# Performance work log

Measured on AMD Instinct MI355X. Metric: run time of the kernel, lower is better.

Reference implementation:

```python
import jax, jax.numpy as jnp
import numpy as np

BN_EPS = 1e-5


def setup_inputs() -> dict:
    key = jax.random.key(0)
    ks = jax.random.split(key, 20)
    B, C, T, H, W = 32, 1024, 4, 14, 14
    Ci = C // 2  # inter_channels = 512
    s = lambda fan: 1.0 / np.sqrt(fan)
    inp = {
        "x_body": jax.random.normal(ks[0], (B, C, T, H, W), jnp.float32),
        "x_face": jax.random.normal(ks[1], (B, 512), jnp.float32),
        # 1x1x1 conv projections of the non-local block
        "Wg": jax.random.normal(ks[2], (Ci, C), jnp.float32) * s(C),
        "bg": jnp.zeros((Ci,), jnp.float32),
        "Wth": jax.random.normal(ks[3], (Ci, C), jnp.float32) * s(C),
        "bth": jnp.zeros((Ci,), jnp.float32),
        "Wph": jax.random.normal(ks[4], (Ci, C), jnp.float32) * s(C),
        "bph": jnp.zeros((Ci,), jnp.float32),
        # output projection W + BatchNorm (inference stats)
        "Ww": jax.random.normal(ks[5], (C, Ci), jnp.float32) * s(Ci),
        "bw": jnp.zeros((C,), jnp.float32),
        "bn_gamma": jax.random.normal(ks[6], (C,), jnp.float32) * 0.1 + 1.0,
        "bn_beta": jax.random.normal(ks[7], (C,), jnp.float32) * 0.1,
        "bn_mean": jax.random.normal(ks[8], (C,), jnp.float32) * 0.1,
        "bn_var": jax.random.uniform(ks[9], (C,), jnp.float32, 0.5, 1.5),
        # FC head
        "W1": jax.random.normal(ks[10], (512, 1024), jnp.float32) * s(1024),
        "b1": jnp.zeros((512,), jnp.float32),
        "W2": jax.random.normal(ks[11], (2, 1024), jnp.float32) * s(1024),
        "b2": jnp.zeros((2,), jnp.float32),
    }
    return inp


def reference(x_body, x_face, Wg, bg, Wth, bth, Wph, bph, Ww, bw,
              bn_gamma, bn_beta, bn_mean, bn_var, W1, b1, W2, b2):
    B, C, T, H, W = x_body.shape
    N = T * H * W  # 784 spatial-temporal positions
    xf = x_body.reshape(B, C, N)

    # embedded-Gaussian non-local block (1x1x1 convs == channel matmuls)
    g_x = jnp.einsum('ic,bcn->bin', Wg, xf) + bg[:, None]      # [B,Ci,N]
    theta = jnp.einsum('ic,bcn->bni', Wth, xf) + bth[None, None, :]  # [B,N,Ci]
    phi = jnp.einsum('ic,bcn->bin', Wph, xf) + bph[:, None]    # [B,Ci,N]
    f = jnp.einsum('bni,bim->bnm', theta, phi)                 # [B,N,N]
    attn = jax.nn.softmax(f, axis=-1)
    y = jnp.einsum('bnm,bim->bin', attn, g_x)                  # [B,Ci,N]

    # W conv back to C channels + BatchNorm (eval) + residual
    wy = jnp.einsum('ci,bin->bcn', Ww, y) + bw[:, None]        # [B,C,N]
    inv = bn_gamma / jnp.sqrt(bn_var + BN_EPS)
    wy = wy * inv[:, None] + (bn_beta - bn_mean * inv)[:, None]
    z = wy + xf                                                # residual

    # adaptive avg pool to (1,1,1) == mean over N, then FC head
    pooled = jnp.mean(z, axis=-1)                              # [B,C]
    h = pooled @ W1.T + b1                                     # [B,512]
    cat = jnp.concatenate([h, x_face], axis=1)                 # [B,1024]
    out = cat @ W2.T + b2                                      # [B,2]
    return out
```

## Files before the change

### kernel.cpp

```cpp
#include <hip/hip_runtime.h>

typedef unsigned short u16;
typedef float f32x4 __attribute__((ext_vector_type(4)));
typedef short s16x8 __attribute__((ext_vector_type(8)));

#define NB 32
#define NC 1024
#define CI 512
#define NN 784
#define NPAD 896
#define M3 1536

#define OFF_XBT   0ull
#define OFF_WCAT  58720256ull
#define OFF_PROJ  61865984ull
#define OFF_ABAR  138985472ull
#define OFF_XBAR  139085824ull
#define OFF_YBAR  0ull
#define OFF_POOL  65536ull
#define OFF_H     196608ull

__device__ __forceinline__ u16 f2bf(float x) {
    union { float f; unsigned u; } v; v.f = x;
    unsigned r = v.u + 0x7fffu + ((v.u >> 16) & 1u);
    return (u16)(r >> 16);
}
__device__ __forceinline__ float bf2f(u16 h) {
    union { unsigned u; float f; } v; v.u = ((unsigned)h) << 16;
    return v.f;
}
__device__ __forceinline__ void gload16(const u16* g, u16* l) {
    __builtin_amdgcn_global_load_lds(
        (const __attribute__((address_space(1))) unsigned int*)(const void*)g,
        (__attribute__((address_space(3))) unsigned int*)(void*)l,
        16, 0, 0);
}
__device__ __forceinline__ float wred_sum(float s) {
    #pragma unroll
    for (int o = 32; o; o >>= 1) s += __shfl_xor(s, o);
    return s;
}

__global__ void k_cast_w(const float* __restrict__ Wth, const float* __restrict__ Wph,
                         const float* __restrict__ Wg, u16* __restrict__ Wcat) {
    int T = blockIdx.x * 256 + threadIdx.x;
    int e = T * 4;
    int row = e >> 10, col = e & 1023;
    const float* src = (row < 512) ? (Wth + (size_t)row * 1024)
                     : (row < 1024) ? (Wph + (size_t)(row - 512) * 1024)
                                    : (Wg + (size_t)(row - 1024) * 1024);
    float4 v = *(const float4*)(src + col);
    ushort4 o;
    o.x = f2bf(v.x); o.y = f2bf(v.y); o.z = f2bf(v.z); o.w = f2bf(v.w);
    *(ushort4*)(Wcat + e) = o;
}

__global__ void k_tcast(const float* __restrict__ xb, u16* __restrict__ xbT,
                        float* __restrict__ xbar) {
    __shared__ float tile[32][33];
    int b = blockIdx.z, c0 = blockIdx.y * 32, n0 = blockIdx.x * 32;
    int t = threadIdx.x, j = t & 31, r0 = t >> 5;
    const float* xp = xb + ((size_t)b * NC + c0) * NN;
    #pragma unroll
    for (int rr = r0; rr < 32; rr += 8) {
        int n = n0 + j;
        tile[rr][j] = (n < NN) ? xp[(size_t)rr * NN + n] : 0.f;
    }
    __syncthreads();
    if (t < 32) {
        float s = 0.f;
        #pragma unroll
        for (int q = 0; q < 32; ++q) s += tile[t][q];
        atomicAdd(&xbar[b * NC + c0 + t], s);
    }
    #pragma unroll
    for (int rr = r0; rr < 32; rr += 8) {
        int n = n0 + rr;
        if (n < NN) xbT[((size_t)b * NPAD + n)* NC + c0 + j] = f2bf(tile[j][rr]);
    }
}

__global__ __launch_bounds__(256) void k_gemm(
        const u16* __restrict__ xbT, const u16* __restrict__ Wcat,
        const float* __restrict__ bth, const float* __restrict__ bph,
        const float* __restrict__ bg, u16* __restrict__ proj) {
    __shared__ u16 At[128 * 32];
    __shared__ u16 Bt[128 * 32];
    int b = blockIdx.z, nt = blockIdx.x, mt = blockIdx.y;
    int t = threadIdx.x, w = t >> 6, l = t & 63;
    int wn = w & 1, wm = w >> 1;
    const u16* Ag = xbT + (size_t)b * NPAD * NC + (size_t)nt * 128 * NC;
    const u16* Bg = Wcat + (size_t)mt * 128 * NC;
    int lrow = l >> 2;
    int cg = ((l & 3) ^ ((l >> 3) & 3)) * 8;
    int lc = l & 15, lr = l >> 4;
    int sA = (lr ^ ((lc >> 1) & 3)) * 8;
    f32x4 acc[4][4] = {};
    for (int kt = 0; kt < 32; ++kt) {
        int k0 = kt * 32;
        int s0 = w * 2, s1 = w * 2 + 1;
        gload16(Ag + (size_t)(s0 * 16 + lrow) * NC + k0 + cg, At + s0 * 512);
        gload16(Ag + (size_t)(s1 * 16 + lrow) * NC + k0 + cg, At + s1 * 512);
        gload16(Bg + (size_t)(s0 * 16 + lrow) * NC + k0 + cg, Bt + s0 * 512);
        gload16(Bg + (size_t)(s1 * 16 + lrow) * NC + k0 + cg, Bt + s1 * 512);
        __syncthreads();
        s16x8 af[4], bf_[4];
        #pragma unroll
        for (int i = 0; i < 4; ++i)
            af[i] = *(const s16x8*)&At[(wn * 64 + i * 16 + lc) * 32 + sA];
        #pragma unroll
        for (int jj = 0; jj < 4; ++jj)
            bf_[jj] = *(const s16x8*)&Bt[(wm * 64 + jj * 16 + lc) * 32 + sA];
        #pragma unroll
        for (int i = 0; i < 4; ++i)
            #pragma unroll
            for (int jj = 0; jj < 4; ++jj)
                acc[i][jj] = __builtin_amdgcn_mfma_f32_16x16x32_bf16(af[i], bf_[jj], acc[i][jj], 0, 0, 0);
        __syncthreads();
    }
    size_t ob = (size_t)b * NN * M3;
    #pragma unroll
    for (int jj = 0; jj < 4; ++jj) {
        int m = mt * 128 + wm * 64 + jj * 16 + lc;
        float bv = (m < 512) ? bth[m] : (m < 1024) ? bph[m - 512] : bg[m - 1024];
        #pragma unroll
        for (int i = 0; i < 4; ++i) {
            int nbase = nt * 128 + wn * 64 + i * 16 + lr * 4;
            #pragma unroll
            for (int r = 0; r < 4; ++r) {
                int n = nbase + r;
                if (n < NN) proj[ob + (size_t)n * M3 + m] = f2bf(acc[i][jj][r] + bv);
            }
        }
    }
}

__global__ __launch_bounds__(256) void k_attn(const u16* __restrict__ proj,
                                              float* __restrict__ abar) {
    extern __shared__ char smem[];
    u16* th   = (u16*)smem;
    float* S  = (float*)(smem + 33280);
    float* rmax = (float*)(smem + 134144);
    float* rinv = rmax + 32;
    int nb = blockIdx.x, b = blockIdx.y;
    int n0 = nb * 32;
    int t = threadIdx.x, w = t >> 6, l = t & 63;
    const u16* pb = proj + (size_t)b * NN * M3;
    {
        int row = t >> 3, kb = (t & 7) * 64;
        const u16* src = pb + (size_t)(n0 + row) * M3 + kb;
        u16* dst = th + row * 520 + kb;
        #pragma unroll
        for (int q = 0; q < 8; ++q) *(s16x8*)(dst + q * 8) = *(const s16x8*)(src + q * 8);
    }
    __syncthreads();
    int lc = l & 15, lr = l >> 4, ko = lr * 8;
    for (int mtile = w; mtile < 49; mtile += 4) {
        f32x4 a0 = {0.f, 0.f, 0.f, 0.f}, a1 = {0.f, 0.f, 0.f, 0.f};
        const u16* ph = pb + 512 + (size_t)(mtile * 16 + lc) * M3;
        #pragma unroll
        for (int ks = 0; ks < 16; ++ks) {
            s16x8 bfrag = *(const s16x8*)(ph + ks * 32 + ko);
            s16x8 t0 = *(const s16x8*)(th + lc * 520 + ks * 32 + ko);
            s16x8 t1 = *(const s16x8*)(th + (16 + lc) * 520 + ks * 32 + ko);
            a0 = __builtin_amdgcn_mfma_f32_16x16x32_bf16(t0, bfrag, a0, 0, 0, 0);
            a1 = __builtin_amdgcn_mfma_f32_16x16x32_bf16(t1, bfrag, a1, 0, 0, 0);
        }
        int m = mtile * 16 + lc;
        #pragma unroll
        for (int r = 0; r < 4; ++r) {
            S[(lr * 4 + r) * 788 + m]        = a0[r];
            S[(16 + lr * 4 + r) * 788 + m]   = a1[r];
        }
    }
    __syncthreads();
    for (int r = w; r < 32; r += 4) {
        const float* Sr = S + r * 788;
        float mx = -1e30f;
        for (int m = l; m < NN; m += 64) mx = fmaxf(mx, Sr[m]);
        #pragma unroll
        for (int o = 32; o; o >>= 1) mx = fmaxf(mx, __shfl_xor(mx, o));
        float sm = 0.f;
        for (int m = l; m < NN; m += 64) sm += __expf(Sr[m] - mx);
        sm = wred_sum(sm);
        if (l == 0) { rmax[r] = mx; rinv[r] = 1.f / sm; }
    }
    __syncthreads();
    int nvalid = NN - n0; if (nvalid > 32) nvalid = 32;
    for (int m = t; m < NN; m += 256) {
        float cs = 0.f;
        for (int r = 0; r < nvalid; ++r) cs += __expf(S[r * 788 + m] - rmax[r]) * rinv[r];
        atomicAdd(&abar[b * NN + m], cs);
    }
}

__global__ __launch_bounds__(256) void k_ybar(const u16* __restrict__ proj,
                                              const float* __restrict__ abar,
                                              float* __restrict__ ybar) {
    __shared__ float part[4][CI];
    __shared__ float ab[49];
    int b = blockIdx.y, m0 = blockIdx.x * 49;
    int t = threadIdx.x, r = t >> 6, l = t & 63;
    if (t < 49) ab[t] = abar[b * NN + m0 + t];
    __syncthreads();
    const u16* g = proj + (size_t)b * NN * M3 + 1024;
    float acc[8] = {};
    for (int m = m0 + r; m < m0 + 49; m += 4) {
        float a = ab[m - m0];
        s16x8 v = *(const s16x8*)(g + (size_t)m * M3 + l * 8);
        #pragma unroll
        for (int j = 0; j < 8; ++j) acc[j] += a * bf2f((u16)v[j]);
    }
    #pragma unroll
    for (int j = 0; j < 8; ++j) part[r][l * 8 + j] = acc[j];
    __syncthreads();
    if (r == 0) {
        #pragma unroll
        for (int j = 0; j < 8; ++j) {
            int i = l * 8 + j;
            atomicAdd(&ybar[b * CI + i],
                      part[0][i] + part[1][i] + part[2][i] + part[3][i]);
        }
    }
}

__global__ __launch_bounds__(256) void k_pooled(const float* __restrict__ ybar,
        const float* __restrict__ xbar,
        const float* __restrict__ Ww, const float* __restrict__ bw,
        const float* __restrict__ gamma, const float* __restrict__ beta,
        const float* __restrict__ mean, const float* __restrict__ var,
        float* __restrict__ pooled) {
    __shared__ float yb[CI];
    int b = blockIdx.y, c0 = blockIdx.x * 128;
    int t = threadIdx.x, w = t >> 6, l = t & 63;
    for (int i = t; i < CI; i += 256) yb[i] = ybar[b * CI + i] * (1.f / 784.f);
    __syncthreads();
    for (int c = c0 + w; c < c0 + 128; c += 4) {
        const float* wr = Ww + (size_t)c * CI;
        float s = 0.f;
        #pragma unroll
        for (int q = 0; q < 8; ++q) s += wr[q * 64 + l] * yb[q * 64 + l];
        s = wred_sum(s);
        if (l == 0) {
            float inv = gamma[c] * rsqrtf(var[c] + 1e-5f);
            pooled[b * NC + c] = inv * (s + bw[c]) + beta[c] - mean[c] * inv
                               + xbar[b * NC + c] * (1.f / 784.f);
        }
    }
}

__global__ __launch_bounds__(256) void k_fc1(const float* __restrict__ pooled,
        const float* __restrict__ W1, const float* __restrict__ b1,
        float* __restrict__ h) {
    __shared__ float pb[NC];
    int b = blockIdx.y, j0 = blockIdx.x * 64;
    int t = threadIdx.x, w = t >> 6, l = t & 63;
    for (int i = t; i < NC; i += 256) pb[i] = pooled[b * NC + i];
    __syncthreads();
    for (int j = j0 + w; j < j0 + 64; j += 4) {
        const float* wr = W1 + (size_t)j * NC;
        float s = 0.f;
        #pragma unroll
        for (int q = 0; q < 16; ++q) s += wr[q * 64 + l] * pb[q * 64 + l];
        s = wred_sum(s);
        if (l == 0) h[b * CI + j] = s + b1[j];
    }
}

__global__ __launch_bounds__(128) void k_fc2(const float* __restrict__ h,
        const float* __restrict__ x_face,
        const float* __restrict__ W2, const float* __restrict__ b2,
        float* __restrict__ out) {
    int b = blockIdx.x, t = threadIdx.x, w = t >> 6, l = t & 63;
    const float* wr = W2 + (size_t)w * NC;
    float s = 0.f;
    #pragma unroll
    for (int q = 0; q < 16; ++q) {
        int qq = q * 64 + l;
        float cv = (qq < 512) ? h[b * CI + qq] : x_face[(size_t)b * 512 + qq - 512];
        s += wr[qq] * cv;
    }
    s = wred_sum(s);
    if (l == 0) out[b * 2 + w] = s + b2[w];
}

extern "C" void kernel_launch(void* const* d_in, const int* in_sizes, int n_in,
                              void* d_out, int out_size, void* d_ws, size_t ws_size,
                              hipStream_t stream) {
    const float* x_body = (const float*)d_in[0];
    const float* x_face = (const float*)d_in[1];
    const float* Wg  = (const float*)d_in[2];
    const float* bg  = (const float*)d_in[3];
    const float* Wth = (const float*)d_in[4];
    const float* bth = (const float*)d_in[5];
    const float* Wph = (const float*)d_in[6];
    const float* bph = (const float*)d_in[7];
    const float* Ww  = (const float*)d_in[8];
    const float* bw  = (const float*)d_in[9];
    const float* gamma = (const float*)d_in[10];
    const float* beta  = (const float*)d_in[11];
    const float* mean  = (const float*)d_in[12];
    const float* var   = (const float*)d_in[13];
    const float* W1 = (const float*)d_in[14];
    const float* b1 = (const float*)d_in[15];
    const float* W2 = (const float*)d_in[16];
    const float* b2 = (const float*)d_in[17];
    (void)in_sizes; (void)n_in; (void)out_size; (void)ws_size;

    char* ws = (char*)d_ws;
    u16* xbT   = (u16*)(ws + OFF_XBT);
    u16* Wcat  = (u16*)(ws + OFF_WCAT);
    u16* proj  = (u16*)(ws + OFF_PROJ);
    float* abar = (float*)(ws + OFF_ABAR);
    float* xbar = (float*)(ws + OFF_XBAR);
    float* ybar = (float*)(ws + OFF_YBAR);
    float* pooled = (float*)(ws + OFF_POOL);
    float* hbuf = (float*)(ws + OFF_H);

    hipMemsetAsync(ws + OFF_ABAR, 0, 100352 + 131072, stream);

    k_cast_w<<<1536, 256, 0, stream>>>(Wth, Wph, Wg, Wcat);
    k_tcast<<<dim3(25, 32, 32), 256, 0, stream>>>(x_body, xbT, xbar);
    k_gemm<<<dim3(7, 12, 32), 256, 0, stream>>>(xbT, Wcat, bth, bph, bg, proj);
    hipMemsetAsync(ws + OFF_YBAR, 0, 65536, stream);
    k_attn<<<dim3(25, 32), 256, 134400, stream>>>(proj, abar);
    k_ybar<<<dim3(16, 32), 256, 0, stream>>>(proj, abar, ybar);
    k_pooled<<<dim3(8, 32), 256, 0, stream>>>(ybar, xbar, Ww, bw,
                                              gamma, beta, mean, var, pooled);
    k_fc1<<<dim3(8, 32), 256, 0, stream>>>(pooled, W1, b1, hbuf);
    k_fc2<<<32, 128, 0, stream>>>(hbuf, x_face, W2, b2, (float*)d_out);
}
```

Baseline: 637.6 us.

## Keep attention scores in registers and remap blocks to XCDs by batch

The attention kernel no longer stages the full 32x784 score matrix in shared memory. Each wave keeps its MFMA accumulators in registers and does the softmax max and sum with shuffles plus a small cross-wave shared reduction, which removes about 100KB of LDS per block and should allow more concurrent blocks. Column sums are reduced within the wave before the atomic add. Both the GEMM and attention grids are flattened and remapped so that each XCD handles a contiguous set of batches, which is meant to improve L2 locality. The register-held accumulators (26 f32x4 per lane) raise VGPR pressure and may reduce occupancy.

After: 548.4 us. 1.16x faster.

```diff
diff --git a/kernel.cpp b/kernel.cpp
--- a/kernel.cpp
+++ b/kernel.cpp
@@ -86,7 +86,11 @@
         const float* __restrict__ bg, u16* __restrict__ proj) {
     __shared__ u16 At[128 * 32];
     __shared__ u16 Bt[128 * 32];
-    int b = blockIdx.z, nt = blockIdx.x, mt = blockIdx.y;
+    int orig = blockIdx.x;
+    int xcd = orig & 7, slot = orig >> 3;
+    int b = xcd * 4 + slot / 84;
+    int rem = slot % 84;
+    int nt = rem / 12, mt = rem % 12;
     int t = threadIdx.x, w = t >> 6, l = t & 63;
     int wn = w & 1, wm = w >> 1;
     const u16* Ag = xbT + (size_t)b * NPAD * NC + (size_t)nt * 128 * NC;
@@ -137,12 +141,13 @@
 
 __global__ __launch_bounds__(256) void k_attn(const u16* __restrict__ proj,
                                               float* __restrict__ abar) {
-    extern __shared__ char smem[];
-    u16* th   = (u16*)smem;
-    float* S  = (float*)(smem + 33280);
-    float* rmax = (float*)(smem + 134144);
-    float* rinv = rmax + 32;
-    int nb = blockIdx.x, b = blockIdx.y;
+    __shared__ u16 th[32 * 520];
+    __shared__ float wmax[4][32];
+    __shared__ float wsum[4][32];
+    int orig = blockIdx.x;
+    int xcd = orig & 7, slot = orig >> 3;
+    int b = xcd * 4 + slot / 25;
+    int nb = slot % 25;
     int n0 = nb * 32;
     int t = threadIdx.x, w = t >> 6, l = t & 63;
     const u16* pb = proj + (size_t)b * NN * M3;
@@ -155,42 +160,116 @@
     }
     __syncthreads();
     int lc = l & 15, lr = l >> 4, ko = lr * 8;
-    for (int mtile = w; mtile < 49; mtile += 4) {
-        f32x4 a0 = {0.f, 0.f, 0.f, 0.f}, a1 = {0.f, 0.f, 0.f, 0.f};
-        const u16* ph = pb + 512 + (size_t)(mtile * 16 + lc) * M3;
-        #pragma unroll
-        for (int ks = 0; ks < 16; ++ks) {
-            s16x8 bfrag = *(const s16x8*)(ph + ks * 32 + ko);
-            s16x8 t0 = *(const s16x8*)(th + lc * 520 + ks * 32 + ko);
-            s16x8 t1 = *(const s16x8*)(th + (16 + lc) * 520 + ks * 32 + ko);
-            a0 = __builtin_amdgcn_mfma_f32_16x16x32_bf16(t0, bfrag, a0, 0, 0, 0);
-            a1 = __builtin_amdgcn_mfma_f32_16x16x32_bf16(t1, bfrag, a1, 0, 0, 0);
-        }
-        int m = mtile * 16 + lc;
-        #pragma unroll
-        for (int r = 0; r < 4; ++r) {
-            S[(lr * 4 + r) * 788 + m]        = a0[r];
-            S[(16 + lr * 4 + r) * 788 + m]   = a1[r];
-        }
-    }
-    __syncthreads();
-    for (int r = w; r < 32; r += 4) {
-        const float* Sr = S + r * 788;
-        float mx = -1e30f;
-        for (int m = l; m < NN; m += 64) mx = fmaxf(mx, Sr[m]);
-        #pragma unroll
-        for (int o = 32; o; o >>= 1) mx = fmaxf(mx, __shfl_xor(mx, o));
-        float sm = 0.f;
-        for (int m = l; m < NN; m += 64) sm += __expf(Sr[m] - mx);
-        sm = wred_sum(sm);
-        if (l == 0) { rmax[r] = mx; rinv[r] = 1.f / sm; }
-    }
-    __syncthreads();
-    int nvalid = NN - n0; if (nvalid > 32) nvalid = 32;
-    for (int m = t; m < NN; m += 256) {
-        float cs = 0.f;
-        for (int r = 0; r < nvalid; ++r) cs += __expf(S[r * 788 + m] - rmax[r]) * rinv[r];
-        atomicAdd(&abar[b * NN + m], cs);
+    f32x4 a0[13], a1[13];
+    #pragma unroll
+    for (int it = 0; it < 13; ++it) {
+        a0[it] = (f32x4){0.f, 0.f, 0.f, 0.f};
+        a1[it] = (f32x4){0.f, 0.f, 0.f, 0.f};
+    }
+    #pragma unroll
+    for (int it = 0; it < 13; ++it) {
+        int mtile = w + it * 4;
+        if (mtile < 49) {
+            const u16* ph = pb + 512 + (size_t)(mtile * 16 + lc) * M3 + ko;
+            #pragma unroll
+            for (int ks = 0; ks < 16; ++ks) {
+                s16x8 bfrag = *(const s16x8*)(ph + ks * 32);
+                s16x8 t0 = *(const s16x8*)(th + lc * 520 + ks * 32 + ko);
+                s16x8 t1 = *(const s16x8*)(th + (16 + lc) * 520 + ks * 32 + ko);
+                a0[it] = __builtin_amdgcn_mfma_f32_16x16x32_bf16(t0, bfrag, a0[it], 0, 0, 0);
+                a1[it] = __builtin_amdgcn_mfma_f32_16x16x32_bf16(t1, bfrag, a1[it], 0, 0, 0);
+            }
+        }
+    }
+    float pm0[4], pm1[4];
+    #pragma unroll
+    for (int j = 0; j < 4; ++j) { pm0[j] = -1e30f; pm1[j] = -1e30f; }
+    #pragma unroll
+    for (int it = 0; it < 13; ++it) {
+        if (w + it * 4 < 49) {
+            #pragma unroll
+            for (int j = 0; j < 4; ++j) {
+                pm0[j] = fmaxf(pm0[j], a0[it][j]);
+                pm1[j] = fmaxf(pm1[j], a1[it][j]);
+            }
+        }
+    }
+    #pragma unroll
+    for (int o = 1; o < 16; o <<= 1) {
+        #pragma unroll
+        for (int j = 0; j < 4; ++j) {
+            pm0[j] = fmaxf(pm0[j], __shfl_xor(pm0[j], o));
+            pm1[j] = fmaxf(pm1[j], __shfl_xor(pm1[j], o));
+        }
+    }
+    if (lc == 0) {
+        #pragma unroll
+        for (int j = 0; j < 4; ++j) {
+            wmax[w][lr * 4 + j] = pm0[j];
+            wmax[w][16 + lr * 4 + j] = pm1[j];
+        }
+    }
+    __syncthreads();
+    float mx0[4], mx1[4];
+    #pragma unroll
+    for (int j = 0; j < 4; ++j) {
+        mx0[j] = fmaxf(fmaxf(wmax[0][lr * 4 + j], wmax[1][lr * 4 + j]),
+                       fmaxf(wmax[2][lr * 4 + j], wmax[3][lr * 4 + j]));
+        mx1[j] = fmaxf(fmaxf(wmax[0][16 + lr * 4 + j], wmax[1][16 + lr * 4 + j]),
+                       fmaxf(wmax[2][16 + lr * 4 + j], wmax[3][16 + lr * 4 + j]));
+    }
+    float ps0[4] = {}, ps1[4] = {};
+    #pragma unroll
+    for (int it = 0; it < 13; ++it) {
+        if (w + it * 4 < 49) {
+            #pragma unroll
+            for (int j = 0; j < 4; ++j) {
+                float e0 = __expf(a0[it][j] - mx0[j]);
+                float e1 = __expf(a1[it][j] - mx1[j]);
+                a0[it][j] = e0; ps0[j] += e0;
+                a1[it][j] = e1; ps1[j] += e1;
+            }
+        }
+    }
+    #pragma unroll
+    for (int o = 1; o < 16; o <<= 1) {
+        #pragma unroll
+        for (int j = 0; j < 4; ++j) {
+            ps0[j] += __shfl_xor(ps0[j], o);
+            ps1[j] += __shfl_xor(ps1[j], o);
+        }
+    }
+    if (lc == 0) {
+        #pragma unroll
+        for (int j = 0; j < 4; ++j) {
+            wsum[w][lr * 4 + j] = ps0[j];
+            wsum[w][16 + lr * 4 + j] = ps1[j];
+        }
+    }
+    __syncthreads();
+    float ri0[4], ri1[4];
+    #pragma unroll
+    for (int j = 0; j < 4; ++j) {
+        float s0 = wsum[0][lr * 4 + j] + wsum[1][lr * 4 + j]
+                 + wsum[2][lr * 4 + j] + wsum[3][lr * 4 + j];
+        float s1 = wsum[0][16 + lr * 4 + j] + wsum[1][16 + lr * 4 + j]
+                 + wsum[2][16 + lr * 4 + j] + wsum[3][16 + lr * 4 + j];
+        ri0[j] = (n0 + lr * 4 + j < NN) ? 1.f / s0 : 0.f;
+        ri1[j] = (n0 + 16 + lr * 4 + j < NN) ? 1.f / s1 : 0.f;
+    }
+    #pragma unroll
+    for (int it = 0; it < 13; ++it) {
+        int mtile = w + it * 4;
+        if (mtile < 49) {
+            float cs = 0.f;
+            #pragma unroll
+            for (int j = 0; j < 4; ++j)
+                cs += a0[it][j] * ri0[j] + a1[it][j] * ri1[j];
+            cs += __shfl_xor(cs, 16);
+            cs += __shfl_xor(cs, 32);
+            if (lr == 0)
+                atomicAdd(&abar[b * NN + mtile * 16 + lc], cs);
+        }
     }
 }
 
@@ -321,9 +400,9 @@
 
     k_cast_w<<<1536, 256, 0, stream>>>(Wth, Wph, Wg, Wcat);
     k_tcast<<<dim3(25, 32, 32), 256, 0, stream>>>(x_body, xbT, xbar);
-    k_gemm<<<dim3(7, 12, 32), 256, 0, stream>>>(xbT, Wcat, bth, bph, bg, proj);
+    k_gemm<<<2688, 256, 0, stream>>>(xbT, Wcat, bth, bph, bg, proj);
     hipMemsetAsync(ws + OFF_YBAR, 0, 65536, stream);
-    k_attn<<<dim3(25, 32), 256, 134400, stream>>>(proj, abar);
+    k_attn<<<800, 256, 0, stream>>>(proj, abar);
     k_ybar<<<dim3(16, 32), 256, 0, stream>>>(proj, abar, ybar);
     k_pooled<<<dim3(8, 32), 256, 0, stream>>>(ybar, xbar, Ww, bw,
                                               gamma, beta, mean, var, pooled);
```
